# Kernel optimization log

Measured on AMD Instinct MI355X. Metric: run time of the kernel, lower is better.

The kernel has to match this reference:

```python
import jax, jax.numpy as jnp
import numpy as np

E, S = 32768, 16
H, D_IN, EDGE_IN = 128, 128, 16
N_SRC, N_DST = 20000, 5000
HEADS, LAYERS, NUM_CLASS = 8, 2, 10
DH = H // HEADS


def _layer_norm(x, g, b, eps=1e-5):
    mu = jnp.mean(x, axis=-1, keepdims=True)
    var = jnp.mean((x - mu) ** 2, axis=-1, keepdims=True)
    return (x - mu) * jax.lax.rsqrt(var + eps) * g + b


def _encoder(e, e_mask, Wqkv, bqkv, Wo, bo, ln1_g, ln1_b, W1, b1, W2, b2, ln2_g, ln2_b):
    # e: [E,S,H]; e_mask: [E,S], True = padding. Post-norm encoder (PyTorch default).
    neg = jnp.float32(-1e9)
    for l in range(LAYERS):
        qkv = e @ Wqkv[l] + bqkv[l]                      # [E,S,3H]
        q, k, v = jnp.split(qkv, 3, axis=-1)
        q = q.reshape(E, S, HEADS, DH)
        k = k.reshape(E, S, HEADS, DH)
        v = v.reshape(E, S, HEADS, DH)
        scores = jnp.einsum('eqhd,ekhd->ehqk', q, k) / np.float32(np.sqrt(DH))
        scores = jnp.where(e_mask[:, None, None, :], neg, scores)
        attn = jax.nn.softmax(scores, axis=-1)
        ctx = jnp.einsum('ehqk,ekhd->eqhd', attn, v).reshape(E, S, H)
        e = _layer_norm(e + (ctx @ Wo[l] + bo[l]), ln1_g[l], ln1_b[l])
        ff = jax.nn.relu(e @ W1[l] + b1[l]) @ W2[l] + b2[l]
        e = _layer_norm(e + ff, ln2_g[l], ln2_b[l])
    return e


def _forward(node_features, edge_features, seq_times, subg_norm,
             W_ein, b_ein, enc_Wqkv, enc_bqkv, enc_Wo, enc_bo, enc_ln1_g, enc_ln1_b,
             enc_W1, enc_b1, enc_W2, enc_b2, enc_ln2_g, enc_ln2_b,
             W_eout, b_eout, W_node, b_node, W_fc, b_fc,
             e_len, e_mask, src_ids, dst_ids, layer_nid):
    h = node_features                                             # [N_src, D_IN]
    self_h = h[layer_nid]                                         # [N_dst, D_IN]
    self_h_tmp = jnp.concatenate([self_h, jnp.zeros((N_DST, H), h.dtype)], axis=1) @ W_eout + b_eout
    # message_func: per-edge sequence -> embed -> transformer -> pool -> concat with src h
    e = jnp.concatenate([edge_features, seq_times[..., None]], axis=-1)  # [E,S,EDGE_IN]
    e = jax.nn.relu(e @ W_ein + b_ein)                                   # [E,S,H]
    e = _encoder(e, e_mask, enc_Wqkv, enc_bqkv, enc_Wo, enc_bo,
                 enc_ln1_g, enc_ln1_b, enc_W1, enc_b1, enc_W2, enc_b2, enc_ln2_g, enc_ln2_b)
    valid = (~e_mask).astype(e.dtype)[..., None]
    e = jnp.sum(e * valid, axis=1) / e_len.astype(e.dtype)[:, None]      # masked mean pool [E,H]
    m = jax.nn.relu(jnp.concatenate([h[src_ids], e], axis=1) @ W_eout + b_eout)  # [E,H]
    h_agg = jax.ops.segment_sum(m, dst_ids, num_segments=N_DST)          # ragged mailbox sum
    hh = (h_agg - self_h_tmp) * subg_norm                                # NodeUpdate (train branch)
    z = jax.nn.relu(jnp.concatenate([self_h, hh], axis=1) @ W_node + b_node)
    return z @ W_fc + b_fc                                               # [N_dst, NUM_CLASS]


def setup_inputs() -> dict:
    key = jax.random.key(0)
    ks = jax.random.split(key, 32)
    inp = {}
    inp['node_features'] = jax.random.normal(ks[0], (N_SRC, D_IN), jnp.float32)
    inp['edge_features'] = jax.random.normal(ks[1], (E, S, EDGE_IN - 1), jnp.float32)
    inp['seq_times'] = jax.random.uniform(ks[2], (E, S), jnp.float32)
    e_len = jax.random.randint(ks[3], (E,), 1, S + 1).astype(jnp.int32)
    inp['e_len'] = e_len
    inp['e_mask'] = jnp.arange(S, dtype=jnp.int32)[None, :] >= e_len[:, None]  # True = pad
    inp['src_ids'] = jax.random.randint(ks[4], (E,), 0, N_SRC).astype(jnp.int32)
    inp['dst_ids'] = jax.random.randint(ks[5], (E,), 0, N_DST).astype(jnp.int32)
    inp['layer_nid'] = jax.random.randint(ks[6], (N_DST,), 0, N_SRC).astype(jnp.int32)
    inp['subg_norm'] = jax.random.uniform(ks[7], (N_DST, 1), jnp.float32, minval=0.01, maxval=1.0)

    def lin(k, fi, fo):
        return jax.random.normal(k, (fi, fo), jnp.float32) / np.float32(np.sqrt(fi))

    inp['W_ein'] = lin(ks[8], EDGE_IN, H); inp['b_ein'] = jnp.zeros((H,), jnp.float32)
    inp['enc_Wqkv'] = jax.random.normal(ks[9], (LAYERS, H, 3 * H), jnp.float32) / np.float32(np.sqrt(H))
    inp['enc_bqkv'] = jnp.zeros((LAYERS, 3 * H), jnp.float32)
    inp['enc_Wo'] = jax.random.normal(ks[10], (LAYERS, H, H), jnp.float32) / np.float32(np.sqrt(H))
    inp['enc_bo'] = jnp.zeros((LAYERS, H), jnp.float32)
    inp['enc_ln1_g'] = jnp.ones((LAYERS, H), jnp.float32); inp['enc_ln1_b'] = jnp.zeros((LAYERS, H), jnp.float32)
    inp['enc_W1'] = jax.random.normal(ks[11], (LAYERS, H, H), jnp.float32) / np.float32(np.sqrt(H))
    inp['enc_b1'] = jnp.zeros((LAYERS, H), jnp.float32)
    inp['enc_W2'] = jax.random.normal(ks[12], (LAYERS, H, H), jnp.float32) / np.float32(np.sqrt(H))
    inp['enc_b2'] = jnp.zeros((LAYERS, H), jnp.float32)
    inp['enc_ln2_g'] = jnp.ones((LAYERS, H), jnp.float32); inp['enc_ln2_b'] = jnp.zeros((LAYERS, H), jnp.float32)
    inp['W_eout'] = lin(ks[13], D_IN + H, H); inp['b_eout'] = jnp.zeros((H,), jnp.float32)
    inp['W_node'] = lin(ks[14], D_IN + H, H); inp['b_node'] = jnp.zeros((H,), jnp.float32)
    inp['W_fc'] = lin(ks[15], H, NUM_CLASS); inp['b_fc'] = jnp.zeros((NUM_CLASS,), jnp.float32)
    return inp


def reference(node_features, edge_features, seq_times, e_len, e_mask, src_ids, dst_ids,
              layer_nid, subg_norm, W_ein, b_ein, enc_Wqkv, enc_bqkv, enc_Wo, enc_bo,
              enc_ln1_g, enc_ln1_b, enc_W1, enc_b1, enc_W2, enc_b2, enc_ln2_g, enc_ln2_b,
              W_eout, b_eout, W_node, b_node, W_fc, b_fc):
    return _forward(node_features, edge_features, seq_times, subg_norm,
                    W_ein, b_ein, enc_Wqkv, enc_bqkv, enc_Wo, enc_bo, enc_ln1_g, enc_ln1_b,
                    enc_W1, enc_b1, enc_W2, enc_b2, enc_ln2_g, enc_ln2_b,
                    W_eout, b_eout, W_node, b_node, W_fc, b_fc,
                    e_len, e_mask, src_ids, dst_ids, layer_nid)
```

## Files before the change

### kernel.cpp

```cpp
#include <hip/hip_runtime.h>

typedef __attribute__((ext_vector_type(8))) short bf16x8;
typedef __attribute__((ext_vector_type(4))) short s16x4;
typedef __attribute__((ext_vector_type(4))) float f32x4;

#define E_N      32768
#define N_DST_N  5000
#define NCLS     10

#define OFF_HAGG   0
#define OFF_POOL   2560000
#define OFF_WPACK  10948608

#define PK_QKV(l)  ((l) * 6144)
#define PK_WO(l)   (12288 + (l) * 2048)
#define PK_W1(l)   (16384 + (l) * 2048)
#define PK_W2(l)   (20480 + (l) * 2048)
#define PK_WEOUT   24576
#define PK_WEIN    28672

__device__ __forceinline__ unsigned short f2bf(float f) {
    unsigned int u = __float_as_uint(f);
    u += 0x7fffu + ((u >> 16) & 1u);
    return (unsigned short)(u >> 16);
}

__global__ void pack_weights(const float* __restrict__ Wqkv,
                             const float* __restrict__ Wo,
                             const float* __restrict__ W1,
                             const float* __restrict__ W2,
                             const float* __restrict__ W_eout,
                             const float* __restrict__ W_ein,
                             unsigned short* __restrict__ wpack) {
    int gid = blockIdx.x * 256 + threadIdx.x;
    if (gid >= 233472) return;
    if (gid >= 229376) {
        int li = gid - 229376;
        int j = li & 7, lane = (li >> 3) & 63, t = li >> 9;
        int k = ((lane >> 4) << 3) + j;
        int n = t * 16 + (lane & 15);
        wpack[gid] = (k < 16) ? f2bf(W_ein[k * 128 + n]) : (unsigned short)0;
        return;
    }
    int id = gid;
    const float* src; int K, N, li;
    if (id < 98304)       { src = Wqkv + (id / 49152) * 49152; li = id % 49152; K = 128; N = 384; }
    else if (id < 131072) { id -= 98304;  src = Wo + (id / 16384) * 16384; li = id % 16384; K = 128; N = 128; }
    else if (id < 163840) { id -= 131072; src = W1 + (id / 16384) * 16384; li = id % 16384; K = 128; N = 128; }
    else if (id < 196608) { id -= 163840; src = W2 + (id / 16384) * 16384; li = id % 16384; K = 128; N = 128; }
    else                  { li = id - 196608; src = W_eout; K = 256; N = 128; }
    int j = li & 7, lane = (li >> 3) & 63, rest = li >> 9;
    int ks = K >> 5;
    int kk = rest % ks, t = rest / ks;
    int k = kk * 32 + ((lane >> 4) << 3) + j;
    int n = t * 16 + (lane & 15);
    wpack[gid] = f2bf(src[k * N + n]);
}

__device__ __forceinline__ void layer_norm_reg(
    float res[2][2][4],
    const float gcol[2], const float bcol[2],
    unsigned short (*a_bf)[136],
    float (*psum)[4], float (*psq)[4],
    int w, int c16, int row4)
{
    float sv[2][4], qv[2][4];
#pragma unroll
    for (int rt = 0; rt < 2; ++rt)
#pragma unroll
        for (int r = 0; r < 4; ++r) {
            float x0 = res[rt][0][r], x1 = res[rt][1][r];
            float s = x0 + x1;
            float q = x0 * x0 + x1 * x1;
#pragma unroll
            for (int d = 1; d < 16; d <<= 1) {
                s += __shfl_xor(s, d);
                q += __shfl_xor(q, d);
            }
            sv[rt][r] = s; qv[rt][r] = q;
        }
    if (c16 == 0) {
#pragma unroll
        for (int rt = 0; rt < 2; ++rt)
#pragma unroll
            for (int r = 0; r < 4; ++r) {
                int row = rt * 16 + row4 + r;
                psum[row][w] = sv[rt][r];
                psq[row][w]  = qv[rt][r];
            }
    }
    __syncthreads();
#pragma unroll
    for (int rt = 0; rt < 2; ++rt)
#pragma unroll
        for (int r = 0; r < 4; ++r) {
            int row = rt * 16 + row4 + r;
            float4 S = *(const float4*)&psum[row][0];
            float4 Q = *(const float4*)&psq[row][0];
            float sum = (S.x + S.y) + (S.z + S.w);
            float sq  = (Q.x + Q.y) + (Q.z + Q.w);
            float mu  = sum * (1.f / 128.f);
            float var = sq * (1.f / 128.f) - mu * mu;
            float inv = rsqrtf(var + 1e-5f);
#pragma unroll
            for (int ti = 0; ti < 2; ++ti) {
                float y = (res[rt][ti][r] - mu) * inv * gcol[ti] + bcol[ti];
                res[rt][ti][r] = y;
                a_bf[row][w * 32 + ti * 16 + c16] = f2bf(y);
            }
        }
}

__global__ __launch_bounds__(256, 3) void edge_kernel(
    const float* __restrict__ edge_features,
    const float* __restrict__ seq_times,
    const int*   __restrict__ e_len,
    const float* __restrict__ b_ein,
    const float* __restrict__ bqkv,  const float* __restrict__ bo,
    const float* __restrict__ ln1_g, const float* __restrict__ ln1_b,
    const float* __restrict__ b1,    const float* __restrict__ b2,
    const float* __restrict__ ln2_g, const float* __restrict__ ln2_b,
    const unsigned short* __restrict__ wpack,
    unsigned short* __restrict__ pooled)
{
    __shared__ __align__(16) unsigned short a_bf[32][136];
    __shared__ __align__(16) unsigned short k_bf[32][136];
    __shared__ __align__(16) unsigned short vT[2][128][24];
    __shared__ __align__(16) unsigned short x_bf[32][40];
    __shared__ __align__(16) float psum[32][4];
    __shared__ __align__(16) float psq[32][4];

    const int tid  = threadIdx.x;
    const int e0   = blockIdx.x * 2;
    const int lane = tid & 63;
    const int w    = tid >> 6;
    const int c16  = lane & 15;
    const int g    = lane >> 4;
    const int row4 = g << 2;
    const int kblk = g << 3;
    const int len0 = e_len[e0];
    const int len1 = e_len[e0 + 1];
    const f32x4 z4 = {0.f, 0.f, 0.f, 0.f};

    float res[2][2][4];

    float lnG[2][2][2], lnB[2][2][2];
#pragma unroll
    for (int l = 0; l < 2; ++l)
#pragma unroll
        for (int ti = 0; ti < 2; ++ti) {
            int col = w * 32 + ti * 16 + c16;
            lnG[l][0][ti] = ln1_g[l * 128 + col];
            lnB[l][0][ti] = ln1_b[l * 128 + col];
            lnG[l][1][ti] = ln2_g[l * 128 + col];
            lnB[l][1][ti] = ln2_b[l * 128 + col];
        }

    for (int idx = tid; idx < 1024; idx += 256) {
        int r = idx >> 5, cc = idx & 31;
        int e = r >> 4, s = r & 15;
        float v = 0.f;
        if (cc < 15)       v = edge_features[(e0 + e) * 240 + s * 15 + cc];
        else if (cc == 15) v = seq_times[(e0 + e) * 16 + s];
        x_bf[r][cc] = f2bf(v);
    }
    __syncthreads();

    const bf16x8* WP = (const bf16x8*)wpack;

    {
        bf16x8 axf[2];
#pragma unroll
        for (int rt = 0; rt < 2; ++rt)
            axf[rt] = *(const bf16x8*)&x_bf[rt * 16 + c16][kblk];
#pragma unroll
        for (int ti = 0; ti < 2; ++ti) {
            bf16x8 bw = WP[PK_WEIN + (2 * w + ti) * 64 + lane];
            int col = (2 * w + ti) * 16 + c16;
            float bias = b_ein[col];
#pragma unroll
            for (int rt = 0; rt < 2; ++rt) {
                f32x4 acc = __builtin_amdgcn_mfma_f32_16x16x32_bf16(axf[rt], bw, z4, 0, 0, 0);
#pragma unroll
                for (int r = 0; r < 4; ++r) {
                    float v = fmaxf(acc[r] + bias, 0.f);
                    res[rt][ti][r] = v;
                    a_bf[rt * 16 + row4 + r][col] = f2bf(v);
                }
            }
        }
    }
    __syncthreads();

    for (int l = 0; l < 2; ++l) {
        {
            bf16x8 af[2][4];
#pragma unroll
            for (int rt = 0; rt < 2; ++rt)
#pragma unroll
                for (int kk = 0; kk < 4; ++kk)
                    af[rt][kk] = *(const bf16x8*)&a_bf[rt * 16 + c16][kk * 32 + kblk];
            __syncthreads();
            const bf16x8* B = WP + PK_QKV(l);
#pragma unroll
            for (int seg = 0; seg < 3; ++seg) {
                bf16x8 bq[2][4];
#pragma unroll
                for (int ti = 0; ti < 2; ++ti)
#pragma unroll
                    for (int kk = 0; kk < 4; ++kk)
                        bq[ti][kk] = B[((seg * 8 + 2 * w + ti) * 4 + kk) * 64 + lane];
#pragma unroll
                for (int ti = 0; ti < 2; ++ti) {
                    int col = (2 * w + ti) * 16 + c16;
                    float bias = bqkv[l * 384 + seg * 128 + col];
#pragma unroll
                    for (int rt = 0; rt < 2; ++rt) {
                        f32x4 acc = z4;
#pragma unroll
                        for (int kk = 0; kk < 4; ++kk)
                            acc = __builtin_amdgcn_mfma_f32_16x16x32_bf16(
                                af[rt][kk], bq[ti][kk], acc, 0, 0, 0);
                        if (seg == 0) {
#pragma unroll
                            for (int r = 0; r < 4; ++r)
                                a_bf[rt * 16 + row4 + r][col] = f2bf(acc[r] + bias);
                        } else if (seg == 1) {
#pragma unroll
                            for (int r = 0; r < 4; ++r)
                                k_bf[rt * 16 + row4 + r][col] = f2bf(acc[r] + bias);
                        } else {
                            s16x4 pk;
#pragma unroll
                            for (int r = 0; r < 4; ++r)
                                pk[r] = (short)f2bf(acc[r] + bias);
                            *(s16x4*)&vT[rt][col][row4] = pk;
                        }
                    }
                }
            }
        }
        __syncthreads();

#pragma unroll
        for (int i = 0; i < 4; ++i) {
            int pp = w * 4 + i;
            int e  = pp >> 3;
            int hb = (pp & 7) * 16;
            int er = e * 16;
            int len = e ? len1 : len0;
            bf16x8 kf = {0,0,0,0,0,0,0,0};
            bf16x8 qf = {0,0,0,0,0,0,0,0};
            bf16x8 vf = {0,0,0,0,0,0,0,0};
            if (lane < 32) {
                kf = *(const bf16x8*)&k_bf[er + c16][hb + kblk];
                qf = *(const bf16x8*)&a_bf[er + c16][hb + kblk];
                vf = *(const bf16x8*)&vT[e][hb + c16][kblk];
            }
            f32x4 st = __builtin_amdgcn_mfma_f32_16x16x32_bf16(kf, qf, z4, 0, 0, 0);
            float sv[4]; float mx = -1e30f;
#pragma unroll
            for (int r = 0; r < 4; ++r) {
                sv[r] = st[r] * 0.25f;
                if (4 * g + r < len) mx = fmaxf(mx, sv[r]);
            }
            mx = fmaxf(mx, __shfl_xor(mx, 16));
            mx = fmaxf(mx, __shfl_xor(mx, 32));
            float p[4]; float sum = 0.f;
#pragma unroll
            for (int r = 0; r < 4; ++r) {
                float pe = (4 * g + r < len) ? __expf(sv[r] - mx) : 0.f;
                p[r] = pe; sum += pe;
            }
            sum += __shfl_xor(sum, 16);
            sum += __shfl_xor(sum, 32);
            float inv = __fdividef(1.f, sum);
            unsigned int own0 = (unsigned int)f2bf(p[0] * inv) | ((unsigned int)f2bf(p[1] * inv) << 16);
            unsigned int own1 = (unsigned int)f2bf(p[2] * inv) | ((unsigned int)f2bf(p[3] * inv) << 16);
            unsigned int t0a = (unsigned int)__shfl((int)own0, (lane + 16) & 63);
            unsigned int t1a = (unsigned int)__shfl((int)own1, (lane + 16) & 63);
            unsigned int t0b = (unsigned int)__shfl((int)own0, (lane + 32) & 63);
            unsigned int t1b = (unsigned int)__shfl((int)own1, (lane + 32) & 63);
            union { unsigned int u[4]; bf16x8 v; } pb;
            if (g == 0)      { pb.u[0] = own0; pb.u[1] = own1; pb.u[2] = t0a; pb.u[3] = t1a; }
            else if (g == 1) { pb.u[0] = t0a;  pb.u[1] = t1a;  pb.u[2] = t0b; pb.u[3] = t1b; }
            else             { pb.u[0] = 0; pb.u[1] = 0; pb.u[2] = 0; pb.u[3] = 0; }
            f32x4 ct = __builtin_amdgcn_mfma_f32_16x16x32_bf16(vf, pb.v, z4, 0, 0, 0);
            s16x4 cpk;
#pragma unroll
            for (int r = 0; r < 4; ++r) cpk[r] = (short)f2bf(ct[r]);
            *(s16x4*)&a_bf[er + c16][hb + 4 * g] = cpk;
        }
        __syncthreads();

        {
            bf16x8 af[2][4];
#pragma unroll
            for (int rt = 0; rt < 2; ++rt)
#pragma unroll
                for (int kk = 0; kk < 4; ++kk)
                    af[rt][kk] = *(const bf16x8*)&a_bf[rt * 16 + c16][kk * 32 + kblk];
            const bf16x8* B = WP + PK_WO(l);
            bf16x8 bw[2][4];
#pragma unroll
            for (int ti = 0; ti < 2; ++ti)
#pragma unroll
                for (int kk = 0; kk < 4; ++kk)
                    bw[ti][kk] = B[((2 * w + ti) * 4 + kk) * 64 + lane];
#pragma unroll
            for (int ti = 0; ti < 2; ++ti) {
                int col = (2 * w + ti) * 16 + c16;
                float bias = bo[l * 128 + col];
#pragma unroll
                for (int rt = 0; rt < 2; ++rt) {
                    f32x4 acc = z4;
#pragma unroll
                    for (int kk = 0; kk < 4; ++kk)
                        acc = __builtin_amdgcn_mfma_f32_16x16x32_bf16(
                            af[rt][kk], bw[ti][kk], acc, 0, 0, 0);
#pragma unroll
                    for (int r = 0; r < 4; ++r)
                        res[rt][ti][r] += acc[r] + bias;
                }
            }
        }
        layer_norm_reg(res, lnG[l][0], lnB[l][0], a_bf, psum, psq, w, c16, row4);
        __syncthreads();

        {
            bf16x8 af[2][4];
#pragma unroll
            for (int rt = 0; rt < 2; ++rt)
#pragma unroll
                for (int kk = 0; kk < 4; ++kk)
                    af[rt][kk] = *(const bf16x8*)&a_bf[rt * 16 + c16][kk * 32 + kblk];
            const bf16x8* B = WP + PK_W1(l);
            bf16x8 bw[2][4];
#pragma unroll
            for (int ti = 0; ti < 2; ++ti)
#pragma unroll
                for (int kk = 0; kk < 4; ++kk)
                    bw[ti][kk] = B[((2 * w + ti) * 4 + kk) * 64 + lane];
            f32x4 acc2[2][2];
#pragma unroll
            for (int ti = 0; ti < 2; ++ti)
#pragma unroll
                for (int rt = 0; rt < 2; ++rt) {
                    f32x4 acc = z4;
#pragma unroll
                    for (int kk = 0; kk < 4; ++kk)
                        acc = __builtin_amdgcn_mfma_f32_16x16x32_bf16(
                            af[rt][kk], bw[ti][kk], acc, 0, 0, 0);
                    acc2[ti][rt] = acc;
                }
            __syncthreads();
#pragma unroll
            for (int ti = 0; ti < 2; ++ti) {
                int col = (2 * w + ti) * 16 + c16;
                float bias = b1[l * 128 + col];
#pragma unroll
                for (int rt = 0; rt < 2; ++rt)
#pragma unroll
                    for (int r = 0; r < 4; ++r)
                        a_bf[rt * 16 + row4 + r][col] =
                            f2bf(fmaxf(acc2[ti][rt][r] + bias, 0.f));
            }
        }
        __syncthreads();

        {
            bf16x8 af[2][4];
#pragma unroll
            for (int rt = 0; rt < 2; ++rt)
#pragma unroll
                for (int kk = 0; kk < 4; ++kk)
                    af[rt][kk] = *(const bf16x8*)&a_bf[rt * 16 + c16][kk * 32 + kblk];
            const bf16x8* B = WP + PK_W2(l);
            bf16x8 bw[2][4];
#pragma unroll
            for (int ti = 0; ti < 2; ++ti)
#pragma unroll
                for (int kk = 0; kk < 4; ++kk)
                    bw[ti][kk] = B[((2 * w + ti) * 4 + kk) * 64 + lane];
#pragma unroll
            for (int ti = 0; ti < 2; ++ti) {
                int col = (2 * w + ti) * 16 + c16;
                float bias = b2[l * 128 + col];
#pragma unroll
                for (int rt = 0; rt < 2; ++rt) {
                    f32x4 acc = z4;
#pragma unroll
                    for (int kk = 0; kk < 4; ++kk)
                        acc = __builtin_amdgcn_mfma_f32_16x16x32_bf16(
                            af[rt][kk], bw[ti][kk], acc, 0, 0, 0);
#pragma unroll
                    for (int r = 0; r < 4; ++r)
                        res[rt][ti][r] += acc[r] + bias;
                }
            }
        }
        layer_norm_reg(res, lnG[l][1], lnB[l][1], a_bf, psum, psq, w, c16, row4);
        __syncthreads();
    }

#pragma unroll
    for (int rt = 0; rt < 2; ++rt) {
        int len = rt ? len1 : len0;
        float fln = (float)len;
#pragma unroll
        for (int ti = 0; ti < 2; ++ti) {
            float s = 0.f;
#pragma unroll
            for (int r = 0; r < 4; ++r)
                if (row4 + r < len) s += res[rt][ti][r];
            s += __shfl_xor(s, 16);
            s += __shfl_xor(s, 32);
            if (lane < 16)
                pooled[(e0 + rt) * 128 + w * 32 + ti * 16 + c16] = f2bf(s / fln);
        }
    }
}

__global__ __launch_bounds__(256) void edge_out_kernel(
    const float* __restrict__ node_features,
    const int* __restrict__ src_ids, const int* __restrict__ dst_ids,
    const unsigned short* __restrict__ pooled,
    const unsigned short* __restrict__ wpack,
    const float* __restrict__ b_eout,
    float* __restrict__ h_agg)
{
    __shared__ __align__(16) unsigned short a2[16][264];
    __shared__ int dst_s[16];
    const int tid = threadIdx.x, lane = tid & 63, w = tid >> 6;
    const int e0 = blockIdx.x * 16;

    {
        int r = tid >> 4, cm = tid & 15;
        int e = e0 + r;
        int src = src_ids[e];
#pragma unroll
        for (int m = 0; m < 8; ++m) {
            int col = cm + 16 * m;
            a2[r][col] = f2bf(node_features[src * 128 + col]);
        }
#pragma unroll
        for (int m = 0; m < 8; ++m) {
            int col = cm + 16 * m;
            a2[r][128 + col] = pooled[e * 128 + col];
        }
        if (tid < 16) dst_s[tid] = dst_ids[e0 + tid];
    }
    __syncthreads();

    const int c16 = lane & 15, row4 = (lane >> 4) << 2, kblk = (lane >> 4) << 3;
    bf16x8 af[8];
#pragma unroll
    for (int kk = 0; kk < 8; ++kk)
        af[kk] = *(const bf16x8*)&a2[c16][kk * 32 + kblk];
    const bf16x8* B = (const bf16x8*)wpack + PK_WEOUT;
#pragma unroll
    for (int ti = 0; ti < 2; ++ti) {
        int t = w * 2 + ti;
        f32x4 acc = {0.f, 0.f, 0.f, 0.f};
#pragma unroll
        for (int kk = 0; kk < 8; ++kk)
            acc = __builtin_amdgcn_mfma_f32_16x16x32_bf16(
                af[kk], B[(t * 8 + kk) * 64 + lane], acc, 0, 0, 0);
        int col = t * 16 + c16;
        float bias = b_eout[col];
#pragma unroll
        for (int r = 0; r < 4; ++r) {
            int row = row4 + r;
            float v = fmaxf(acc[r] + bias, 0.f);
            atomicAdd(&h_agg[dst_s[row] * 128 + col], v);
        }
    }
}

__global__ __launch_bounds__(128) void node_kernel(
    const float* __restrict__ node_features,
    const int*   __restrict__ layer_nid,
    const float* __restrict__ subg_norm,
    const float* __restrict__ h_agg,
    const float* __restrict__ W_eout, const float* __restrict__ b_eout,
    const float* __restrict__ W_node, const float* __restrict__ b_node,
    const float* __restrict__ W_fc,   const float* __restrict__ b_fc,
    float* __restrict__ out)
{
    __shared__ float sh[128];
    __shared__ float hh[128];
    __shared__ float z[128];

    const int n   = blockIdx.x;
    const int tid = threadIdx.x;
    const int nid = layer_nid[n];
    const float norm = subg_norm[n];

    sh[tid] = node_features[nid * 128 + tid];
    __syncthreads();

    float acc = 0.f;
#pragma unroll 4
    for (int k = 0; k < 128; ++k)
        acc = fmaf(sh[k], W_eout[k * 128 + tid], acc);
    acc += b_eout[tid];
    hh[tid] = (h_agg[n * 128 + tid] - acc) * norm;
    __syncthreads();

    float za = 0.f;
#pragma unroll 4
    for (int k = 0; k < 128; ++k)
        za = fmaf(sh[k], W_node[k * 128 + tid], za);
#pragma unroll 4
    for (int k = 0; k < 128; ++k)
        za = fmaf(hh[k], W_node[(128 + k) * 128 + tid], za);
    za += b_node[tid];
    z[tid] = fmaxf(za, 0.f);
    __syncthreads();

    if (tid < NCLS) {
        float o = 0.f;
#pragma unroll 4
        for (int k = 0; k < 128; ++k)
            o = fmaf(z[k], W_fc[k * NCLS + tid], o);
        out[n * NCLS + tid] = o + b_fc[tid];
    }
}


extern "C" void kernel_launch(void* const* d_in, const int* in_sizes, int n_in,
                              void* d_out, int out_size, void* d_ws, size_t ws_size,
                              hipStream_t stream) {
    const float* node_features = (const float*)d_in[0];
    const float* edge_features = (const float*)d_in[1];
    const float* seq_times     = (const float*)d_in[2];
    const int*   e_len         = (const int*)d_in[3];
    const int*   src_ids       = (const int*)d_in[5];
    const int*   dst_ids       = (const int*)d_in[6];
    const int*   layer_nid     = (const int*)d_in[7];
    const float* subg_norm     = (const float*)d_in[8];
    const float* W_ein  = (const float*)d_in[9];
    const float* b_ein  = (const float*)d_in[10];
    const float* Wqkv   = (const float*)d_in[11];
    const float* bqkv   = (const float*)d_in[12];
    const float* Wo     = (const float*)d_in[13];
    const float* bo     = (const float*)d_in[14];
    const float* ln1_g  = (const float*)d_in[15];
    const float* ln1_b  = (const float*)d_in[16];
    const float* W1     = (const float*)d_in[17];
    const float* b1     = (const float*)d_in[18];
    const float* W2     = (const float*)d_in[19];
    const float* b2     = (const float*)d_in[20];
    const float* ln2_g  = (const float*)d_in[21];
    const float* ln2_b  = (const float*)d_in[22];
    const float* W_eout = (const float*)d_in[23];
    const float* b_eout = (const float*)d_in[24];
    const float* W_node = (const float*)d_in[25];
    const float* b_node = (const float*)d_in[26];
    const float* W_fc   = (const float*)d_in[27];
    const float* b_fc   = (const float*)d_in[28];

    float*          h_agg  = (float*)((char*)d_ws + OFF_HAGG);
    unsigned short* pooled = (unsigned short*)((char*)d_ws + OFF_POOL);
    unsigned short* wpack  = (unsigned short*)((char*)d_ws + OFF_WPACK);

    pack_weights<<<912, 256, 0, stream>>>(Wqkv, Wo, W1, W2, W_eout, W_ein, wpack);
    hipMemsetAsync(h_agg, 0, (size_t)N_DST_N * 128 * sizeof(float), stream);

    edge_kernel<<<E_N / 2, 256, 0, stream>>>(
        edge_features, seq_times, e_len,
        b_ein, bqkv, bo, ln1_g, ln1_b, b1, b2, ln2_g, ln2_b,
        wpack, pooled);

    edge_out_kernel<<<E_N / 16, 256, 0, stream>>>(
        node_features, src_ids, dst_ids, pooled, wpack, b_eout, h_agg);

    node_kernel<<<N_DST_N, 128, 0, stream>>>(
        node_features, layer_nid, subg_norm, h_agg,
        W_eout, b_eout, W_node, b_node, W_fc, b_fc, (float*)d_out);
}
```

Before: 827.7 us.

## Use native bf16 conversion, alias x_bf with vT, raise occupancy bound

Replaces the hand-written round-to-nearest-even float-to-bf16 bit trick with the HIP bf16 intrinsics, including a packed two-value conversion that may map to a hardware pack instruction on gfx950. The x_bf staging buffer now shares LDS with vT through a union, which is safe because x_bf is only used before the first QKV projection. Launch bounds are raised from 3 to 5 blocks per CU. Together these cut LDS footprint and conversion instruction count to allow more resident blocks, at the risk of register spills under the tighter register budget.

```diff
diff --git a/kernel.cpp b/kernel.cpp
--- a/kernel.cpp
+++ b/kernel.cpp
@@ -1,4 +1,5 @@
 #include <hip/hip_runtime.h>
+#include <hip/hip_bf16.h>
 
 typedef __attribute__((ext_vector_type(8))) short bf16x8;
 typedef __attribute__((ext_vector_type(4))) short s16x4;
@@ -20,9 +21,16 @@
 #define PK_WEIN    28672
 
 __device__ __forceinline__ unsigned short f2bf(float f) {
-    unsigned int u = __float_as_uint(f);
-    u += 0x7fffu + ((u >> 16) & 1u);
-    return (unsigned short)(u >> 16);
+    __hip_bfloat16 h = __float2bfloat16(f);
+    unsigned short u;
+    __builtin_memcpy(&u, &h, 2);
+    return u;
+}
+__device__ __forceinline__ unsigned int f2bf2(float lo, float hi) {
+    __hip_bfloat162 h = __float22bfloat162_rn(make_float2(lo, hi));
+    unsigned int u;
+    __builtin_memcpy(&u, &h, 4);
+    return u;
 }
 
 __global__ void pack_weights(const float* __restrict__ Wqkv,
@@ -111,7 +119,7 @@
         }
 }
 
-__global__ __launch_bounds__(256, 3) void edge_kernel(
+__global__ __launch_bounds__(256, 5) void edge_kernel(
     const float* __restrict__ edge_features,
     const float* __restrict__ seq_times,
     const int*   __restrict__ e_len,
@@ -125,8 +133,10 @@
 {
     __shared__ __align__(16) unsigned short a_bf[32][136];
     __shared__ __align__(16) unsigned short k_bf[32][136];
-    __shared__ __align__(16) unsigned short vT[2][128][24];
-    __shared__ __align__(16) unsigned short x_bf[32][40];
+    __shared__ __align__(16) union VX {
+        unsigned short vT[2][128][24];
+        unsigned short x_bf[32][40];
+    } vx;
     __shared__ __align__(16) float psum[32][4];
     __shared__ __align__(16) float psq[32][4];
 
@@ -162,7 +172,7 @@
         float v = 0.f;
         if (cc < 15)       v = edge_features[(e0 + e) * 240 + s * 15 + cc];
         else if (cc == 15) v = seq_times[(e0 + e) * 16 + s];
-        x_bf[r][cc] = f2bf(v);
+        vx.x_bf[r][cc] = f2bf(v);
     }
     __syncthreads();
 
@@ -172,7 +182,7 @@
         bf16x8 axf[2];
 #pragma unroll
         for (int rt = 0; rt < 2; ++rt)
-            axf[rt] = *(const bf16x8*)&x_bf[rt * 16 + c16][kblk];
+            axf[rt] = *(const bf16x8*)&vx.x_bf[rt * 16 + c16][kblk];
 #pragma unroll
         for (int ti = 0; ti < 2; ++ti) {
             bf16x8 bw = WP[PK_WEIN + (2 * w + ti) * 64 + lane];
@@ -230,11 +240,10 @@
                             for (int r = 0; r < 4; ++r)
                                 k_bf[rt * 16 + row4 + r][col] = f2bf(acc[r] + bias);
                         } else {
-                            s16x4 pk;
-#pragma unroll
-                            for (int r = 0; r < 4; ++r)
-                                pk[r] = (short)f2bf(acc[r] + bias);
-                            *(s16x4*)&vT[rt][col][row4] = pk;
+                            union { unsigned int u[2]; s16x4 v; } pk;
+                            pk.u[0] = f2bf2(acc[0] + bias, acc[1] + bias);
+                            pk.u[1] = f2bf2(acc[2] + bias, acc[3] + bias);
+                            *(s16x4*)&vx.vT[rt][col][row4] = pk.v;
                         }
                     }
                 }
@@ -255,7 +264,7 @@
             if (lane < 32) {
                 kf = *(const bf16x8*)&k_bf[er + c16][hb + kblk];
                 qf = *(const bf16x8*)&a_bf[er + c16][hb + kblk];
-                vf = *(const bf16x8*)&vT[e][hb + c16][kblk];
+                vf = *(const bf16x8*)&vx.vT[e][hb + c16][kblk];
             }
             f32x4 st = __builtin_amdgcn_mfma_f32_16x16x32_bf16(kf, qf, z4, 0, 0, 0);
             float sv[4]; float mx = -1e30f;
@@ -275,8 +284,8 @@
             sum += __shfl_xor(sum, 16);
             sum += __shfl_xor(sum, 32);
             float inv = __fdividef(1.f, sum);
-            unsigned int own0 = (unsigned int)f2bf(p[0] * inv) | ((unsigned int)f2bf(p[1] * inv) << 16);
-            unsigned int own1 = (unsigned int)f2bf(p[2] * inv) | ((unsigned int)f2bf(p[3] * inv) << 16);
+            unsigned int own0 = f2bf2(p[0] * inv, p[1] * inv);
+            unsigned int own1 = f2bf2(p[2] * inv, p[3] * inv);
             unsigned int t0a = (unsigned int)__shfl((int)own0, (lane + 16) & 63);
             unsigned int t1a = (unsigned int)__shfl((int)own1, (lane + 16) & 63);
             unsigned int t0b = (unsigned int)__shfl((int)own0, (lane + 32) & 63);
@@ -286,10 +295,10 @@
             else if (g == 1) { pb.u[0] = t0a;  pb.u[1] = t1a;  pb.u[2] = t0b; pb.u[3] = t1b; }
             else             { pb.u[0] = 0; pb.u[1] = 0; pb.u[2] = 0; pb.u[3] = 0; }
             f32x4 ct = __builtin_amdgcn_mfma_f32_16x16x32_bf16(vf, pb.v, z4, 0, 0, 0);
-            s16x4 cpk;
-#pragma unroll
-            for (int r = 0; r < 4; ++r) cpk[r] = (short)f2bf(ct[r]);
-            *(s16x4*)&a_bf[er + c16][hb + 4 * g] = cpk;
+            union { unsigned int u[2]; s16x4 v; } cpk;
+            cpk.u[0] = f2bf2(ct[0], ct[1]);
+            cpk.u[1] = f2bf2(ct[2], ct[3]);
+            *(s16x4*)&a_bf[er + c16][hb + 4 * g] = cpk.v;
         }
         __syncthreads();
 
```

New measurement: 929.7 us. +12.3%, slower.
